# Performance work log

Hardware: AMD Instinct MI355X
Metric: run time of the kernel (lower is better)

Reference implementation:

```python
import jax, jax.numpy as jnp
import numpy as np

# ---- hash-grid encoder constants (instant-ngp / tiny-cuda-nn style) ----
L = 24          # nr_levels (hard-coded in Density.__init__)
F = 2           # features per level -> output_dim = 48
T = 2 ** 19     # hashmap size per level
BASE_RES = 16
FINEST_RES = 2048
_b = np.exp(np.log(FINEST_RES / BASE_RES) / (L - 1))
RES = np.floor(BASE_RES * _b ** np.arange(L)).astype(np.float32)  # [L]
PRIMES = np.array([1, 2654435761, 805459861], dtype=np.uint32)
OFFS = np.array([[(i >> d) & 1 for d in range(3)] for i in range(8)], dtype=np.int32)  # [8,3] cube corners


def hash_encode(points, hash_table, bb_sides):
    """points [N,3] in [-bb/2, bb/2]; hash_table [L,T,F] -> [N, L*F]."""
    x = jnp.clip(points / bb_sides + 0.5, 0.0, 1.0)  # normalize to unit cube

    def level_fn(_, lv):
        tbl, res = lv                     # tbl [T,F], res scalar
        pos = x * res                     # [N,3]
        i0 = jnp.floor(pos)
        w = pos - i0                      # [N,3] trilinear weights
        corner = i0.astype(jnp.uint32)[:, None, :] + jnp.asarray(OFFS, jnp.uint32)[None]  # [N,8,3]
        hp = corner * jnp.asarray(PRIMES)[None, None, :]
        h = (hp[..., 0] ^ hp[..., 1] ^ hp[..., 2]) & jnp.uint32(T - 1)  # [N,8]
        wts = jnp.where(jnp.asarray(OFFS, bool)[None], w[:, None, :], 1.0 - w[:, None, :]).prod(-1)  # [N,8]
        feat = tbl[h]                     # gather [N,8,F]
        return 0, (wts[..., None] * feat).sum(axis=1)  # [N,F]

    _, feats = jax.lax.scan(level_fn, 0, (hash_table, jnp.asarray(RES)))  # [L,N,F]
    return jnp.transpose(feats, (1, 0, 2)).reshape(points.shape[0], L * F)


def setup_inputs() -> dict:
    key = jax.random.key(0)
    ks = jax.random.split(key, 8)
    N = 1048576
    points = jax.random.uniform(ks[0], (N, 3), dtype=jnp.float32) * 2.0 - 1.0  # in bb [-1,1]^3
    bb_sides = jnp.full((3,), 2.0, dtype=jnp.float32)
    hash_table = jax.random.uniform(ks[1], (L, T, F), dtype=jnp.float32, minval=-1e-4, maxval=1e-4)
    d_enc, d_h, d_out = L * F, 64, 33  # 1 density + 32 geom feats
    w1 = jax.random.normal(ks[2], (d_enc, d_h), dtype=jnp.float32) / np.sqrt(d_enc)
    b1 = jnp.zeros((d_h,), jnp.float32)
    w2 = jax.random.normal(ks[3], (d_h, d_h), dtype=jnp.float32) / np.sqrt(d_h)
    b2 = jnp.zeros((d_h,), jnp.float32)
    w3 = jax.random.normal(ks[4], (d_h, d_out), dtype=jnp.float32) / np.sqrt(d_h)
    b3 = jnp.zeros((d_out,), jnp.float32)
    return {"points": points, "bb_sides": bb_sides, "hash_table": hash_table,
            "w1": w1, "b1": b1, "w2": w2, "b2": b2, "w3": w3, "b3": b3}


def reference(points, bb_sides, hash_table, w1, b1, w2, b2, w3, b3):
    enc = hash_encode(points, hash_table, bb_sides)        # [N,48]
    h = jax.nn.relu(enc @ w1 + b1)
    h = jax.nn.relu(h @ w2 + b2)
    out = h @ w3 + b3                                      # [N,33], last layer linear
    density = jax.nn.softplus(out[:, 0:1])                 # [N,1]
    geom_feat = out[:, 1:]                                 # [N,32]
    return density, geom_feat
```

## Files before the change

kernel.cpp:

```cpp
#include <hip/hip_runtime.h>
#include <math.h>

#define TSZ 524288u
#define TMASK 524287u

#define WPACK 5808
#define ENC_OFF 8192

struct ResTab { float v[24]; };

typedef __attribute__((ext_vector_type(8))) short frag_ab;
typedef __attribute__((ext_vector_type(4))) float frag_cd;

union FU { uint4 u; frag_ab f; };

static __device__ __forceinline__ frag_ab ldfrag(const unsigned int* p) {
    FU x; x.u = *(const uint4*)p; return x.f;
}
static __device__ __forceinline__ float bf2f(unsigned int u) {
    return __uint_as_float(u << 16);
}
static __device__ __forceinline__ unsigned short f2bf(float f) {
    unsigned int u = __float_as_uint(f);
    unsigned int r = (u + 0x7fffu + ((u >> 16) & 1u)) >> 16;
    return (unsigned short)r;
}
static __device__ __forceinline__ float lo16(unsigned int d) { return __uint_as_float(d << 16); }
static __device__ __forceinline__ float hi16(unsigned int d) { return __uint_as_float(d & 0xffff0000u); }

template<bool F32>
static __device__ __forceinline__ float ld(const void* p, int i) {
    if constexpr (F32) return ((const float*)p)[i];
    else return bf2f((unsigned int)((const unsigned short*)p)[i]);
}

static __device__ __forceinline__ frag_cd mfma(frag_ab a, frag_ab b, frag_cd c) {
    return __builtin_amdgcn_mfma_f32_16x16x32_bf16(a, b, c, 0, 0, 0);
}

template<bool F32>
static __device__ __forceinline__ unsigned int encode_one(
    float x0, float x1, float x2, float rr, const void* tbl, int l)
{
    float p0 = x0 * rr, p1 = x1 * rr, p2 = x2 * rr;
    float f0 = floorf(p0), f1 = floorf(p1), f2 = floorf(p2);
    float w0 = p0 - f0, w1v = p1 - f1, w2v = p2 - f2;
    unsigned int i0 = (unsigned int)f0, i1 = (unsigned int)f1, i2 = (unsigned int)f2;
    unsigned int ax0 = i0, ax1 = i0 + 1u;
    unsigned int ay0 = i1 * 2654435761u, ay1 = ay0 + 2654435761u;
    unsigned int az0 = i2 * 805459861u,  az1 = az0 + 805459861u;
    unsigned int h0 = (ax0 ^ ay0 ^ az0) & TMASK;
    unsigned int h1 = (ax1 ^ ay0 ^ az0) & TMASK;
    unsigned int h2 = (ax0 ^ ay1 ^ az0) & TMASK;
    unsigned int h3 = (ax1 ^ ay1 ^ az0) & TMASK;
    unsigned int h4 = (ax0 ^ ay0 ^ az1) & TMASK;
    unsigned int h5 = (ax1 ^ ay0 ^ az1) & TMASK;
    unsigned int h6 = (ax0 ^ ay1 ^ az1) & TMASK;
    unsigned int h7 = (ax1 ^ ay1 ^ az1) & TMASK;

    float g0l, g0h, g1l, g1h, g2l, g2h, g3l, g3h;
    float g4l, g4h, g5l, g5h, g6l, g6h, g7l, g7h;
    if constexpr (F32) {
        const float2* lt = (const float2*)tbl + (size_t)l * TSZ;
        float2 d0 = lt[h0], d1 = lt[h1], d2 = lt[h2], d3 = lt[h3];
        float2 d4 = lt[h4], d5 = lt[h5], d6 = lt[h6], d7 = lt[h7];
        g0l = d0.x; g0h = d0.y; g1l = d1.x; g1h = d1.y;
        g2l = d2.x; g2h = d2.y; g3l = d3.x; g3h = d3.y;
        g4l = d4.x; g4h = d4.y; g5l = d5.x; g5h = d5.y;
        g6l = d6.x; g6h = d6.y; g7l = d7.x; g7h = d7.y;
    } else {
        const unsigned int* lt = (const unsigned int*)tbl + (size_t)l * TSZ;
        unsigned int d0 = lt[h0], d1 = lt[h1], d2 = lt[h2], d3 = lt[h3];
        unsigned int d4 = lt[h4], d5 = lt[h5], d6 = lt[h6], d7 = lt[h7];
        g0l = lo16(d0); g0h = hi16(d0); g1l = lo16(d1); g1h = hi16(d1);
        g2l = lo16(d2); g2h = hi16(d2); g3l = lo16(d3); g3h = hi16(d3);
        g4l = lo16(d4); g4h = hi16(d4); g5l = lo16(d5); g5h = hi16(d5);
        g6l = lo16(d6); g6h = hi16(d6); g7l = lo16(d7); g7h = hi16(d7);
    }

    float v0 = 1.f - w0, v1 = 1.f - w1v, v2 = 1.f - w2v;
    float wy0z0 = v1 * v2,  wy1z0 = w1v * v2;
    float wy0z1 = v1 * w2v, wy1z1 = w1v * w2v;
    float c0 = v0 * wy0z0, c1 = w0 * wy0z0, c2 = v0 * wy1z0, c3 = w0 * wy1z0;
    float c4 = v0 * wy0z1, c5 = w0 * wy0z1, c6 = v0 * wy1z1, c7 = w0 * wy1z1;
    float e0 = c0 * g0l + c1 * g1l + c2 * g2l + c3 * g3l
             + c4 * g4l + c5 * g5l + c6 * g6l + c7 * g7l;
    float e1 = c0 * g0h + c1 * g1h + c2 * g2h + c3 * g3h
             + c4 * g4h + c5 * g5h + c6 * g6h + c7 * g7h;
    return (unsigned int)f2bf(e0) | (((unsigned int)f2bf(e1)) << 16);
}

static __device__ __forceinline__ void hidden_layer(
    const unsigned int* Wu, const float* Bv, frag_ab A[4][2],
    unsigned int* sAu, int wv, int li, int qq)
{
#pragma unroll
    for (int nt = 0; nt < 4; ++nt) {
        frag_ab Bf0 = ldfrag(&Wu[(((nt * 16 + li) * 8) + (qq ^ (li & 7))) * 4]);
        frag_ab Bf1 = ldfrag(&Wu[(((nt * 16 + li) * 8) + ((4 + qq) ^ (li & 7))) * 4]);
        float bias = Bv[nt * 16 + li];
#pragma unroll
        for (int m = 0; m < 4; ++m) {
            frag_cd c = {0.f, 0.f, 0.f, 0.f};
            c = mfma(A[m][0], Bf0, c);
            c = mfma(A[m][1], Bf1, c);
            int dst4 = ((wv * 4 + m) * 2 + (nt >> 1)) * 64 + ((nt * 2 + (li >> 3)) & 3) * 16;
#pragma unroll
            for (int r = 0; r < 4; ++r) {
                float v = fmaxf(c[r] + bias, 0.f);
                unsigned int mybf = f2bf(v);
                unsigned int oth = (unsigned int)(unsigned short)__shfl_xor((int)mybf, 1, 64);
                if (!(li & 1))
                    sAu[(dst4 + qq * 4 + r) * 4 + ((li & 7) >> 1)] = mybf | (oth << 16);
            }
        }
    }
}

static __device__ __forceinline__ void mlp_tail(
    const unsigned int* Wf1, const unsigned int* Wf2, const unsigned int* Wf3,
    const float* Bf1, const float* Bf2, const float* Bf3,
    float* out, int N, unsigned int* sAu)
{
    const int t  = threadIdx.x;
    const int ln = t & 63;
    const int wv = t >> 6;
    const int li = t & 15;
    const int qq = ln >> 4;

    frag_ab A[4][2];
#pragma unroll
    for (int m = 0; m < 4; ++m)
#pragma unroll
        for (int ks = 0; ks < 2; ++ks)
            A[m][ks] = ldfrag(&sAu[((((wv * 4 + m) * 2) + ks) * 64 + ln) * 4]);

    hidden_layer(Wf1, Bf1, A, sAu, wv, li, qq);
    __syncthreads();
#pragma unroll
    for (int m = 0; m < 4; ++m)
#pragma unroll
        for (int ks = 0; ks < 2; ++ks)
            A[m][ks] = ldfrag(&sAu[((((wv * 4 + m) * 2) + ks) * 64 + ln) * 4]);

    hidden_layer(Wf2, Bf2, A, sAu, wv, li, qq);
    __syncthreads();
#pragma unroll
    for (int m = 0; m < 4; ++m)
#pragma unroll
        for (int ks = 0; ks < 2; ++ks)
            A[m][ks] = ldfrag(&sAu[((((wv * 4 + m) * 2) + ks) * 64 + ln) * 4]);

#pragma unroll
    for (int nt = 0; nt < 3; ++nt) {
        frag_ab Bf0 = ldfrag(&Wf3[(((nt * 16 + li) * 8) + (qq ^ (li & 7))) * 4]);
        frag_ab Bf1 = ldfrag(&Wf3[(((nt * 16 + li) * 8) + ((4 + qq) ^ (li & 7))) * 4]);
        float bias = Bf3[nt * 16 + li];
        int col = nt * 16 + li;
#pragma unroll
        for (int m = 0; m < 4; ++m) {
            frag_cd c = {0.f, 0.f, 0.f, 0.f};
            c = mfma(A[m][0], Bf0, c);
            c = mfma(A[m][1], Bf1, c);
#pragma unroll
            for (int r = 0; r < 4; ++r) {
                float v = c[r] + bias;
                unsigned int mybf = f2bf(v);
                unsigned int oth = (unsigned int)(unsigned short)__shfl_xor((int)mybf, 1, 64);
                if (!(li & 1) && col < 33)
                    sAu[wv * 2048 + (m * 16 + qq * 4 + r) * 17 + (col >> 1)] = mybf | (oth << 16);
            }
        }
    }

    __syncthreads();

    {
        int bStart = blockIdx.x * 256;
        {
            unsigned int u0 = sAu[(t >> 6) * 2048 + (t & 63) * 17];
            float v0 = bf2f(u0 & 0xffffu);
            float sp = (v0 > 20.f) ? v0 : log1pf(expf(v0));
            if (bStart + t < N) out[bStart + t] = sp;
        }
        float* og = out + N + (size_t)bStart * 32;
#pragma unroll
        for (int i = 0; i < 8; ++i) {
            int j  = i * 1024 + t * 4;
            int pt = j >> 5;
            int c  = j & 31;
            const unsigned int* rp = &sAu[(pt >> 6) * 2048 + (pt & 63) * 17];
            unsigned int a0 = rp[(c >> 1)];
            unsigned int a1 = rp[(c >> 1) + 1];
            unsigned int a2 = rp[(c >> 1) + 2];
            float4 q;
            q.x = bf2f(a0 >> 16);
            q.y = bf2f(a1 & 0xffffu);
            q.z = bf2f(a1 >> 16);
            q.w = bf2f(a2 & 0xffffu);
            if (bStart + pt < N) *(float4*)&og[j] = q;
        }
    }
}

static __device__ __forceinline__ void zero_pad_rows(unsigned int* sAu) {
    const int t  = threadIdx.x;
    const int wv = t >> 6;
    const int mt = (t >> 4) & 3;
    const int li = t & 15;
    uint4 z; z.x = 0u; z.y = 0u; z.z = 0u; z.w = 0u;
    int u2 = ((wv * 4 + mt) * 2 + 1) * 64 + 2 * 16 + li;
    int u3 = ((wv * 4 + mt) * 2 + 1) * 64 + 3 * 16 + li;
    *(uint4*)&sAu[u2 * 4] = z;
    *(uint4*)&sAu[u3 * 4] = z;
}


template<bool F32>
static __device__ __forceinline__ void gather_body(
    const void* points, const void* bb, const void* tbl,
    unsigned int* enc, int N, size_t Np, int nB2, const ResTab& rt)
{
    const int t = threadIdx.x;
    int l  = blockIdx.x / nB2;
    int bx = blockIdx.x - l * nB2;
    int p0 = bx * 512 + t;
    int p1 = p0 + 256;
    int pc0 = (p0 < N) ? p0 : (N - 1);
    int pc1 = (p1 < N) ? p1 : (N - 1);

    float ax = ld<F32>(points, pc0 * 3 + 0);
    float ay = ld<F32>(points, pc0 * 3 + 1);
    float az = ld<F32>(points, pc0 * 3 + 2);
    float bx_ = ld<F32>(points, pc1 * 3 + 0);
    float by_ = ld<F32>(points, pc1 * 3 + 1);
    float bz_ = ld<F32>(points, pc1 * 3 + 2);
    float ib0 = 1.f / ld<F32>(bb, 0);
    float ib1 = 1.f / ld<F32>(bb, 1);
    float ib2 = 1.f / ld<F32>(bb, 2);
    float xa0 = fminf(fmaxf(ax * ib0 + 0.5f, 0.f), 1.f);
    float xa1 = fminf(fmaxf(ay * ib1 + 0.5f, 0.f), 1.f);
    float xa2 = fminf(fmaxf(az * ib2 + 0.5f, 0.f), 1.f);
    float xb0 = fminf(fmaxf(bx_ * ib0 + 0.5f, 0.f), 1.f);
    float xb1 = fminf(fmaxf(by_ * ib1 + 0.5f, 0.f), 1.f);
    float xb2 = fminf(fmaxf(bz_ * ib2 + 0.5f, 0.f), 1.f);

    const float rr = rt.v[l];
    unsigned int pk0 = encode_one<F32>(xa0, xa1, xa2, rr, tbl, l);
    unsigned int pk1 = encode_one<F32>(xb0, xb1, xb2, rr, tbl, l);
    __builtin_nontemporal_store(pk0, &enc[(size_t)l * Np + p0]);
    __builtin_nontemporal_store(pk1, &enc[(size_t)l * Np + p1]);
}

__global__ __launch_bounds__(256) void ngp_gather(
    const void* __restrict__ points, const void* __restrict__ bb,
    const void* __restrict__ tbl, unsigned int* __restrict__ enc,
    int N, unsigned long long Np, int nB2, ResTab rt)
{
    bool isF32 = (((const unsigned int*)bb)[0] == 0x40000000u);
    if (isF32) gather_body<true>(points, bb, tbl, enc, N, (size_t)Np, nB2, rt);
    else       gather_body<false>(points, bb, tbl, enc, N, (size_t)Np, nB2, rt);
}

__global__ __launch_bounds__(256, 4) void ngp_mlp(
    const unsigned int* __restrict__ enc, const unsigned int* __restrict__ wp,
    float* __restrict__ out, int N, unsigned long long Np)
{
    __shared__ unsigned int sAu[8192];

    const int t  = threadIdx.x;
    const int wv = t >> 6;
    const int mt = (t >> 4) & 3;
    const int li = t & 15;

    zero_pad_rows(sAu);

    const int rowBase = ((wv * 4 + mt) * 2) * 64 + li;
#pragma unroll
    for (int l = 0; l < 24; ++l) {
        unsigned int pk = enc[(size_t)l * Np + blockIdx.x * 256 + t];
        sAu[(rowBase + (l >> 4) * 64 + ((l >> 2) & 3) * 16) * 4 + (l & 3)] = pk;
    }

    __syncthreads();

    mlp_tail(wp, wp + 2048, wp + 4096,
             (const float*)(wp + 5632), (const float*)(wp + 5696),
             (const float*)(wp + 5760), out, N, sAu);
}

template<bool F32>
static __device__ __forceinline__ void pack_body(
    const void* w1, const void* b1, const void* w2, const void* b2,
    const void* w3, const void* b3, unsigned int* wp)
{
    const int t = threadIdx.x;
    unsigned int* W1 = wp;
    unsigned int* W2 = wp + 2048;
    unsigned int* W3 = wp + 4096;
    float* B1 = (float*)(wp + 5632);
    float* B2 = (float*)(wp + 5696);
    float* B3 = (float*)(wp + 5760);

    for (int idx = t; idx < 2048; idx += 256) {
        int n = idx & 63, k0 = (idx >> 6) * 2;
        unsigned int lo1 = (k0     < 48) ? f2bf(ld<F32>(w1, k0 * 64 + n))       : 0u;
        unsigned int hi1 = (k0 + 1 < 48) ? f2bf(ld<F32>(w1, (k0 + 1) * 64 + n)) : 0u;
        unsigned int lo2 = f2bf(ld<F32>(w2, k0 * 64 + n));
        unsigned int hi2 = f2bf(ld<F32>(w2, (k0 + 1) * 64 + n));
        int dst = (n * 8 + ((k0 >> 3) ^ (n & 7))) * 4 + ((k0 & 7) >> 1);
        W1[dst] = lo1 | (hi1 << 16);
        W2[dst] = lo2 | (hi2 << 16);
    }
    for (int idx = t; idx < 1536; idx += 256) {
        int n = idx >> 5, k0 = (idx & 31) * 2;
        unsigned int lo = (n < 33) ? f2bf(ld<F32>(w3, k0 * 33 + n))       : 0u;
        unsigned int hi = (n < 33) ? f2bf(ld<F32>(w3, (k0 + 1) * 33 + n)) : 0u;
        int dst = (n * 8 + ((k0 >> 3) ^ (n & 7))) * 4 + ((k0 & 7) >> 1);
        W3[dst] = lo | (hi << 16);
    }
    if (t < 64) { B1[t] = ld<F32>(b1, t); B2[t] = ld<F32>(b2, t); }
    if (t < 48) B3[t] = (t < 33) ? ld<F32>(b3, t) : 0.f;
}

__global__ void pack_weights(
    const void* __restrict__ bb,
    const void* __restrict__ w1, const void* __restrict__ b1,
    const void* __restrict__ w2, const void* __restrict__ b2,
    const void* __restrict__ w3, const void* __restrict__ b3,
    unsigned int* __restrict__ wp)
{
    bool isF32 = (((const unsigned int*)bb)[0] == 0x40000000u);
    if (isF32) pack_body<true>(w1, b1, w2, b2, w3, b3, wp);
    else       pack_body<false>(w1, b1, w2, b2, w3, b3, wp);
}


template<bool F32>
static __device__ __forceinline__ void body_lds(
    const void* points, const void* bb, const void* tbl,
    const void* w1, const void* b1, const void* w2, const void* b2,
    const void* w3, const void* b3,
    float* out, int N, const ResTab& rt,
    unsigned int* sAu, unsigned int* sW1u, unsigned int* sW2u, unsigned int* sW3u,
    float* sB1, float* sB2, float* sB3)
{
    const int t  = threadIdx.x;
    const int wv = t >> 6;
    const int mt = (t >> 4) & 3;
    const int li = t & 15;

    for (int idx = t; idx < 2048; idx += 256) {
        int n = idx & 63, k0 = (idx >> 6) * 2;
        unsigned int lo1 = (k0     < 48) ? f2bf(ld<F32>(w1, k0 * 64 + n))       : 0u;
        unsigned int hi1 = (k0 + 1 < 48) ? f2bf(ld<F32>(w1, (k0 + 1) * 64 + n)) : 0u;
        unsigned int lo2 = f2bf(ld<F32>(w2, k0 * 64 + n));
        unsigned int hi2 = f2bf(ld<F32>(w2, (k0 + 1) * 64 + n));
        int dst = (n * 8 + ((k0 >> 3) ^ (n & 7))) * 4 + ((k0 & 7) >> 1);
        sW1u[dst] = lo1 | (hi1 << 16);
        sW2u[dst] = lo2 | (hi2 << 16);
    }
    for (int idx = t; idx < 1536; idx += 256) {
        int n = idx >> 5, k0 = (idx & 31) * 2;
        unsigned int lo = (n < 33) ? f2bf(ld<F32>(w3, k0 * 33 + n))       : 0u;
        unsigned int hi = (n < 33) ? f2bf(ld<F32>(w3, (k0 + 1) * 33 + n)) : 0u;
        int dst = (n * 8 + ((k0 >> 3) ^ (n & 7))) * 4 + ((k0 & 7) >> 1);
        sW3u[dst] = lo | (hi << 16);
    }
    if (t < 64) { sB1[t] = ld<F32>(b1, t); sB2[t] = ld<F32>(b2, t); }
    if (t < 48) sB3[t] = (t < 33) ? ld<F32>(b3, t) : 0.f;

    zero_pad_rows(sAu);

    int p  = blockIdx.x * 256 + t;
    int pc = (p < N) ? p : (N - 1);
    float ptx = ld<F32>(points, pc * 3 + 0);
    float pty = ld<F32>(points, pc * 3 + 1);
    float ptz = ld<F32>(points, pc * 3 + 2);
    float x0 = fminf(fmaxf(ptx / ld<F32>(bb, 0) + 0.5f, 0.f), 1.f);
    float x1 = fminf(fmaxf(pty / ld<F32>(bb, 1) + 0.5f, 0.f), 1.f);
    float x2 = fminf(fmaxf(ptz / ld<F32>(bb, 2) + 0.5f, 0.f), 1.f);

    const int rowBase = ((wv * 4 + mt) * 2) * 64 + li;

#pragma unroll 4
    for (int l = 0; l < 24; ++l) {
        unsigned int pk = encode_one<F32>(x0, x1, x2, rt.v[l], tbl, l);
        sAu[(rowBase + (l >> 4) * 64 + ((l >> 2) & 3) * 16) * 4 + (l & 3)] = pk;
    }

    __syncthreads();

    mlp_tail(sW1u, sW2u, sW3u, sB1, sB2, sB3, out, N, sAu);
}

__global__ __launch_bounds__(256, 2) void ngp_fused(
    const void* __restrict__ points, const void* __restrict__ bb,
    const void* __restrict__ tbl,
    const void* __restrict__ w1, const void* __restrict__ b1,
    const void* __restrict__ w2, const void* __restrict__ b2,
    const void* __restrict__ w3, const void* __restrict__ b3,
    float* __restrict__ out, int N, ResTab rt)
{
    __shared__ unsigned int sAu[8192];
    __shared__ unsigned int sW1u[2048];
    __shared__ unsigned int sW2u[2048];
    __shared__ unsigned int sW3u[1536];
    __shared__ float sB1[64], sB2[64], sB3[48];

    bool isF32 = (((const unsigned int*)bb)[0] == 0x40000000u);
    if (isF32)
        body_lds<true>(points, bb, tbl, w1, b1, w2, b2, w3, b3, out, N, rt,
                       sAu, sW1u, sW2u, sW3u, sB1, sB2, sB3);
    else
        body_lds<false>(points, bb, tbl, w1, b1, w2, b2, w3, b3, out, N, rt,
                        sAu, sW1u, sW2u, sW3u, sB1, sB2, sB3);
}

extern "C" void kernel_launch(void* const* d_in, const int* in_sizes, int n_in,
                              void* d_out, int out_size, void* d_ws, size_t ws_size,
                              hipStream_t stream) {
    const void* points = nullptr; const void* bb = nullptr; const void* tbl = nullptr;
    const void* w1 = nullptr; const void* b1 = nullptr;
    const void* w2 = nullptr; const void* b2 = nullptr;
    const void* w3 = nullptr; const void* b3 = nullptr;

    int iTbl = -1, iPts = -1;
    long sTbl = -1, sPts = -1;
    for (int i = 0; i < n_in; ++i) {
        long s = in_sizes[i];
        if (s > sTbl) { sPts = sTbl; iPts = iTbl; sTbl = s; iTbl = i; }
        else if (s > sPts) { sPts = s; iPts = i; }
    }
    tbl = d_in[iTbl];
    points = d_in[iPts];
    for (int i = 0; i < n_in; ++i) {
        if (i == iTbl || i == iPts) continue;
        int s = in_sizes[i];
        if      (s == 4096) w2 = d_in[i];
        else if (s == 3072) w1 = d_in[i];
        else if (s == 2112) w3 = d_in[i];
        else if (s == 33)   b3 = d_in[i];
        else if (s == 3)    bb = d_in[i];
        else if (s == 64)   { if (!b1) b1 = d_in[i]; else b2 = d_in[i]; }
    }

    int N = (int)(sPts / 3);

    ResTab rt;
    double bexp = exp(log(2048.0 / 16.0) / 23.0);
    for (int l = 0; l < 24; ++l)
        rt.v[l] = (float)floor(16.0 * pow(bexp, (double)l));

    int nb  = (N + 255) / 256;
    int nB2 = (N + 511) / 512;
    unsigned long long Np = (unsigned long long)nB2 * 512;
    size_t need = ((size_t)ENC_OFF + (size_t)24 * Np) * 4;

    if (d_ws && ws_size >= need) {
        unsigned int* wp  = (unsigned int*)d_ws;
        unsigned int* enc = wp + ENC_OFF;
        pack_weights<<<1, 256, 0, stream>>>(bb, w1, b1, w2, b2, w3, b3, wp);
        ngp_gather<<<nB2 * 24, 256, 0, stream>>>(points, bb, tbl, enc, N, Np, nB2, rt);
        int nbm = (int)(Np / 256);
        ngp_mlp<<<nbm, 256, 0, stream>>>(enc, wp, (float*)d_out, N, Np);
    } else {
        ngp_fused<<<nb, 256, 0, stream>>>(points, bb, tbl, w1, b1, w2, b2, w3, b3,
                                          (float*)d_out, N, rt);
    }
}
```

Measured before the change: 885.0 us.

## Split hash-grid gather into coarse multi-level kernel plus per-level launches

Replaces the single level-major gather launch with one kernel that encodes the 8 coarse levels per point in a loop, followed by 16 separate per-level launches for the fine levels. This keeps each fine level's 4 MB table slice hot in cache during its own launch and amortises point loads for the small coarse tables. It also replaces shuffle-and-pack bf16 stores in the MLP with direct 16-bit shared-memory stores. The cost is 16 extra kernel launches, with points reloaded and bb divisions recomputed in each one.

```diff
diff --git a/kernel.cpp b/kernel.cpp
--- a/kernel.cpp
+++ b/kernel.cpp
@@ -94,6 +94,7 @@
     const unsigned int* Wu, const float* Bv, frag_ab A[4][2],
     unsigned int* sAu, int wv, int li, int qq)
 {
+    unsigned short* sAs = (unsigned short*)sAu;
 #pragma unroll
     for (int nt = 0; nt < 4; ++nt) {
         frag_ab Bf0 = ldfrag(&Wu[(((nt * 16 + li) * 8) + (qq ^ (li & 7))) * 4]);
@@ -108,10 +109,7 @@
 #pragma unroll
             for (int r = 0; r < 4; ++r) {
                 float v = fmaxf(c[r] + bias, 0.f);
-                unsigned int mybf = f2bf(v);
-                unsigned int oth = (unsigned int)(unsigned short)__shfl_xor((int)mybf, 1, 64);
-                if (!(li & 1))
-                    sAu[(dst4 + qq * 4 + r) * 4 + ((li & 7) >> 1)] = mybf | (oth << 16);
+                sAs[((dst4 + qq * 4 + r) * 4 + ((li & 7) >> 1)) * 2 + (li & 1)] = f2bf(v);
             }
         }
     }
@@ -151,24 +149,25 @@
         for (int ks = 0; ks < 2; ++ks)
             A[m][ks] = ldfrag(&sAu[((((wv * 4 + m) * 2) + ks) * 64 + ln) * 4]);
 
-#pragma unroll
-    for (int nt = 0; nt < 3; ++nt) {
-        frag_ab Bf0 = ldfrag(&Wf3[(((nt * 16 + li) * 8) + (qq ^ (li & 7))) * 4]);
-        frag_ab Bf1 = ldfrag(&Wf3[(((nt * 16 + li) * 8) + ((4 + qq) ^ (li & 7))) * 4]);
-        float bias = Bf3[nt * 16 + li];
-        int col = nt * 16 + li;
-#pragma unroll
-        for (int m = 0; m < 4; ++m) {
-            frag_cd c = {0.f, 0.f, 0.f, 0.f};
-            c = mfma(A[m][0], Bf0, c);
-            c = mfma(A[m][1], Bf1, c);
-#pragma unroll
-            for (int r = 0; r < 4; ++r) {
-                float v = c[r] + bias;
-                unsigned int mybf = f2bf(v);
-                unsigned int oth = (unsigned int)(unsigned short)__shfl_xor((int)mybf, 1, 64);
-                if (!(li & 1) && col < 33)
-                    sAu[wv * 2048 + (m * 16 + qq * 4 + r) * 17 + (col >> 1)] = mybf | (oth << 16);
+    {
+        unsigned short* sAs = (unsigned short*)sAu;
+#pragma unroll
+        for (int nt = 0; nt < 3; ++nt) {
+            frag_ab Bf0 = ldfrag(&Wf3[(((nt * 16 + li) * 8) + (qq ^ (li & 7))) * 4]);
+            frag_ab Bf1 = ldfrag(&Wf3[(((nt * 16 + li) * 8) + ((4 + qq) ^ (li & 7))) * 4]);
+            float bias = Bf3[nt * 16 + li];
+            int col = nt * 16 + li;
+#pragma unroll
+            for (int m = 0; m < 4; ++m) {
+                frag_cd c = {0.f, 0.f, 0.f, 0.f};
+                c = mfma(A[m][0], Bf0, c);
+                c = mfma(A[m][1], Bf1, c);
+#pragma unroll
+                for (int r = 0; r < 4; ++r) {
+                    float v = c[r] + bias;
+                    if (col < 34)
+                        sAs[(wv * 2048 + (m * 16 + qq * 4 + r) * 17 + (col >> 1)) * 2 + (li & 1)] = f2bf(v);
+                }
             }
         }
     }
@@ -217,49 +216,64 @@
 
 
 template<bool F32>
-static __device__ __forceinline__ void gather_body(
+static __device__ __forceinline__ void gather_coarse_body(
     const void* points, const void* bb, const void* tbl,
-    unsigned int* enc, int N, size_t Np, int nB2, const ResTab& rt)
+    unsigned int* enc, int N, size_t Np, const ResTab& rt)
 {
     const int t = threadIdx.x;
-    int l  = blockIdx.x / nB2;
-    int bx = blockIdx.x - l * nB2;
-    int p0 = bx * 512 + t;
-    int p1 = p0 + 256;
-    int pc0 = (p0 < N) ? p0 : (N - 1);
-    int pc1 = (p1 < N) ? p1 : (N - 1);
-
-    float ax = ld<F32>(points, pc0 * 3 + 0);
-    float ay = ld<F32>(points, pc0 * 3 + 1);
-    float az = ld<F32>(points, pc0 * 3 + 2);
-    float bx_ = ld<F32>(points, pc1 * 3 + 0);
-    float by_ = ld<F32>(points, pc1 * 3 + 1);
-    float bz_ = ld<F32>(points, pc1 * 3 + 2);
-    float ib0 = 1.f / ld<F32>(bb, 0);
-    float ib1 = 1.f / ld<F32>(bb, 1);
-    float ib2 = 1.f / ld<F32>(bb, 2);
-    float xa0 = fminf(fmaxf(ax * ib0 + 0.5f, 0.f), 1.f);
-    float xa1 = fminf(fmaxf(ay * ib1 + 0.5f, 0.f), 1.f);
-    float xa2 = fminf(fmaxf(az * ib2 + 0.5f, 0.f), 1.f);
-    float xb0 = fminf(fmaxf(bx_ * ib0 + 0.5f, 0.f), 1.f);
-    float xb1 = fminf(fmaxf(by_ * ib1 + 0.5f, 0.f), 1.f);
-    float xb2 = fminf(fmaxf(bz_ * ib2 + 0.5f, 0.f), 1.f);
-
-    const float rr = rt.v[l];
-    unsigned int pk0 = encode_one<F32>(xa0, xa1, xa2, rr, tbl, l);
-    unsigned int pk1 = encode_one<F32>(xb0, xb1, xb2, rr, tbl, l);
-    __builtin_nontemporal_store(pk0, &enc[(size_t)l * Np + p0]);
-    __builtin_nontemporal_store(pk1, &enc[(size_t)l * Np + p1]);
-}
-
-__global__ __launch_bounds__(256) void ngp_gather(
+    int p  = blockIdx.x * 256 + t;
+    int pc = (p < N) ? p : (N - 1);
+    float ptx = ld<F32>(points, pc * 3 + 0);
+    float pty = ld<F32>(points, pc * 3 + 1);
+    float ptz = ld<F32>(points, pc * 3 + 2);
+    float x0 = fminf(fmaxf(ptx / ld<F32>(bb, 0) + 0.5f, 0.f), 1.f);
+    float x1 = fminf(fmaxf(pty / ld<F32>(bb, 1) + 0.5f, 0.f), 1.f);
+    float x2 = fminf(fmaxf(ptz / ld<F32>(bb, 2) + 0.5f, 0.f), 1.f);
+
+#pragma unroll
+    for (int l = 0; l < 8; ++l) {
+        unsigned int pk = encode_one<F32>(x0, x1, x2, rt.v[l], tbl, l);
+        __builtin_nontemporal_store(pk, &enc[(size_t)l * Np + p]);
+    }
+}
+
+__global__ __launch_bounds__(256) void ngp_gather_coarse(
     const void* __restrict__ points, const void* __restrict__ bb,
     const void* __restrict__ tbl, unsigned int* __restrict__ enc,
-    int N, unsigned long long Np, int nB2, ResTab rt)
+    int N, unsigned long long Np, ResTab rt)
 {
     bool isF32 = (((const unsigned int*)bb)[0] == 0x40000000u);
-    if (isF32) gather_body<true>(points, bb, tbl, enc, N, (size_t)Np, nB2, rt);
-    else       gather_body<false>(points, bb, tbl, enc, N, (size_t)Np, nB2, rt);
+    if (isF32) gather_coarse_body<true>(points, bb, tbl, enc, N, (size_t)Np, rt);
+    else       gather_coarse_body<false>(points, bb, tbl, enc, N, (size_t)Np, rt);
+}
+
+template<bool F32>
+static __device__ __forceinline__ void gather_lvl_body(
+    const void* points, const void* bb, const void* tbl,
+    unsigned int* enc, int N, size_t Np, int l, float rr)
+{
+    const int t = threadIdx.x;
+    int p  = blockIdx.x * 256 + t;
+    int pc = (p < N) ? p : (N - 1);
+    float ptx = ld<F32>(points, pc * 3 + 0);
+    float pty = ld<F32>(points, pc * 3 + 1);
+    float ptz = ld<F32>(points, pc * 3 + 2);
+    float x0 = fminf(fmaxf(ptx / ld<F32>(bb, 0) + 0.5f, 0.f), 1.f);
+    float x1 = fminf(fmaxf(pty / ld<F32>(bb, 1) + 0.5f, 0.f), 1.f);
+    float x2 = fminf(fmaxf(ptz / ld<F32>(bb, 2) + 0.5f, 0.f), 1.f);
+
+    unsigned int pk = encode_one<F32>(x0, x1, x2, rr, tbl, l);
+    __builtin_nontemporal_store(pk, &enc[(size_t)l * Np + p]);
+}
+
+__global__ __launch_bounds__(256) void ngp_gather_lvl(
+    const void* __restrict__ points, const void* __restrict__ bb,
+    const void* __restrict__ tbl, unsigned int* __restrict__ enc,
+    int N, unsigned long long Np, int l, float rr)
+{
+    bool isF32 = (((const unsigned int*)bb)[0] == 0x40000000u);
+    if (isF32) gather_lvl_body<true>(points, bb, tbl, enc, N, (size_t)Np, l, rr);
+    else       gather_lvl_body<false>(points, bb, tbl, enc, N, (size_t)Np, l, rr);
 }
 
 __global__ __launch_bounds__(256, 4) void ngp_mlp(
@@ -452,18 +466,19 @@
     for (int l = 0; l < 24; ++l)
         rt.v[l] = (float)floor(16.0 * pow(bexp, (double)l));
 
-    int nb  = (N + 255) / 256;
-    int nB2 = (N + 511) / 512;
-    unsigned long long Np = (unsigned long long)nB2 * 512;
+    int nb = (N + 255) / 256;
+    unsigned long long Np = (unsigned long long)nb * 256;
     size_t need = ((size_t)ENC_OFF + (size_t)24 * Np) * 4;
 
     if (d_ws && ws_size >= need) {
         unsigned int* wp  = (unsigned int*)d_ws;
         unsigned int* enc = wp + ENC_OFF;
         pack_weights<<<1, 256, 0, stream>>>(bb, w1, b1, w2, b2, w3, b3, wp);
-        ngp_gather<<<nB2 * 24, 256, 0, stream>>>(points, bb, tbl, enc, N, Np, nB2, rt);
-        int nbm = (int)(Np / 256);
-        ngp_mlp<<<nbm, 256, 0, stream>>>(enc, wp, (float*)d_out, N, Np);
+        ngp_gather_coarse<<<nb, 256, 0, stream>>>(points, bb, tbl, enc, N, Np, rt);
+        for (int l = 8; l < 24; ++l)
+            ngp_gather_lvl<<<nb, 256, 0, stream>>>(points, bb, tbl, enc, N, Np,
+                                                   l, rt.v[l]);
+        ngp_mlp<<<nb, 256, 0, stream>>>(enc, wp, (float*)d_out, N, Np);
     } else {
         ngp_fused<<<nb, 256, 0, stream>>>(points, bb, tbl, w1, b1, w2, b2, w3, b3,
                                           (float*)d_out, N, rt);
```

Measured after the change: 886.0 us. About the same (+0.1%).
